# Kernel tuning notes

Measured on AMD Instinct MI355X. Metric: run time of the kernel, lower is better.

Reference implementation:

```python
import jax, jax.numpy as jnp
import numpy as np

RX, RY = 10, 10  # box filter half-widths (Angle == 0 path)


def setup_inputs() -> dict:
    key = jax.random.key(0)
    x = jax.random.normal(key, (8, 1, 2048, 2048), dtype=jnp.float32)
    # Angle == 0: constant all-ones box kernel (1,1,2rx+1,2ry+1), a fixed buffer
    kernelx = jnp.ones((1, 1, 2 * RX + 1, 2 * RY + 1), dtype=jnp.float32)
    return {"x": x, "kernelx": kernelx}


def reference(x, kernelx):
    # circular pad: H by rx (top/bottom), W by ry (left/right), matching
    # F.pad(input, (ry, ry, rx, rx), mode='circular')
    xp = jnp.pad(x, ((0, 0), (0, 0), (RX, RX), (RY, RY)), mode="wrap")
    # valid conv with the box kernel -> output has the original HxW
    out = jax.lax.conv_general_dilated(
        xp, kernelx,
        window_strides=(1, 1),
        padding="VALID",
        dimension_numbers=("NCHW", "OIHW", "NCHW"),
    )
    return out
```

## Files before the change

kernel.cpp:

```cpp
#include <hip/hip_runtime.h>


#define HH 2048
#define WW 2048
#define RAD 10
#define DIAM 21
#define TH 64
#define TW 64
#define CS_W (TW + 2 * RAD)
#define CS_STRIDE (CS_W + 1)

__global__ __launch_bounds__(256) void box_filter_v2(
    const float* __restrict__ x, float* __restrict__ out) {
  __shared__ float sCS[TH * CS_STRIDE];

  const int n = blockIdx.z;
  const int h0 = blockIdx.y * TH;
  const int w0 = blockIdx.x * TW;
  const float* __restrict__ xp = x + (size_t)n * HH * WW;
  float* __restrict__ op = out + (size_t)n * HH * WW;
  const int tid = threadIdx.x;

  for (int t = tid; t < CS_W * 4; t += 256) {
    int c = t % CS_W;
    int g = t / CS_W;
    int gc = (w0 - RAD + c) & (WW - 1);
    int rbase = h0 + 16 * g - RAD;
    float v[36];
#pragma unroll
    for (int k = 0; k < 36; ++k)
      v[k] = xp[(size_t)((rbase + k) & (HH - 1)) * WW + gc];
    float s = 0.f;
#pragma unroll
    for (int k = 0; k < DIAM; ++k) s += v[k];
    sCS[(16 * g) * CS_STRIDE + c] = s;
#pragma unroll
    for (int i = 1; i < 16; ++i) {
      s += v[i + DIAM - 1] - v[i - 1];
      sCS[(16 * g + i) * CS_STRIDE + c] = s;
    }
  }
  __syncthreads();

  {
    int r = tid >> 2;
    int cg = tid & 3;
    const float* csrow = &sCS[r * CS_STRIDE + cg * 16];
    float w[36];
#pragma unroll
    for (int k = 0; k < 36; ++k) w[k] = csrow[k];
    float o[16];
    float s = 0.f;
#pragma unroll
    for (int k = 0; k < DIAM; ++k) s += w[k];
    o[0] = s;
#pragma unroll
    for (int j = 1; j < 16; ++j) {
      s += w[j + DIAM - 1] - w[j - 1];
      o[j] = s;
    }
    float4* dst = (float4*)&op[(size_t)(h0 + r) * WW + w0 + cg * 16];
#pragma unroll
    for (int q = 0; q < 4; ++q)
      dst[q] = make_float4(o[4 * q], o[4 * q + 1], o[4 * q + 2], o[4 * q + 3]);
  }
}

extern "C" void kernel_launch(void* const* d_in, const int* in_sizes, int n_in,
                              void* d_out, int out_size, void* d_ws, size_t ws_size,
                              hipStream_t stream) {
  const float* x = (const float*)d_in[0];
  float* out = (float*)d_out;
  dim3 grid(WW / TW, HH / TH, 8);
  dim3 block(256);
  hipLaunchKernelGGL(box_filter_v2, grid, block, 0, stream, x, out);
}
```

Measured before the change: 261.8 us.

## Widen tile to 128 columns and vectorize vertical pass with float4 loads

The tile width doubles to 128 columns. The vertical sliding-sum pass now loads float4 columns, so each thread handles four columns and the 12-column aligned halo is read with 16-byte loads. The horizontal pass reads shared memory as float4 and computes two 16-wide output groups per thread. This cuts redundant halo reads and the number of scalar global loads, at the cost of much higher register use (36 float4 per thread) and 104 idle threads in the first phase.

```diff
diff --git a/kernel.cpp b/kernel.cpp
--- a/kernel.cpp
+++ b/kernel.cpp
@@ -6,63 +6,73 @@
 #define RAD 10
 #define DIAM 21
 #define TH 64
-#define TW 64
-#define CS_W (TW + 2 * RAD)
-#define CS_STRIDE (CS_W + 1)
+#define TW 128
+#define NC4 38
+#define SSTR 156
 
-__global__ __launch_bounds__(256) void box_filter_v2(
+__global__ __launch_bounds__(256) void box_filter_v3(
     const float* __restrict__ x, float* __restrict__ out) {
-  __shared__ float sCS[TH * CS_STRIDE];
+  __shared__ float sCS[TH * SSTR];
 
   const int n = blockIdx.z;
   const int h0 = blockIdx.y * TH;
   const int w0 = blockIdx.x * TW;
-  const float* __restrict__ xp = x + (size_t)n * HH * WW;
-  float* __restrict__ op = out + (size_t)n * HH * WW;
+  const float* __restrict__ xp = x + (size_t)n * (HH * WW);
+  float* __restrict__ op = out + (size_t)n * (HH * WW);
   const int tid = threadIdx.x;
 
-  for (int t = tid; t < CS_W * 4; t += 256) {
-    int c = t % CS_W;
-    int g = t / CS_W;
-    int gc = (w0 - RAD + c) & (WW - 1);
-    int rbase = h0 + 16 * g - RAD;
-    float v[36];
+  if (tid < NC4 * 4) {
+    const int c4 = tid % NC4;
+    const int g = tid / NC4;
+    const int gc = (w0 - 12 + 4 * c4) & (WW - 1);
+    const int rbase = h0 + 16 * g - RAD;
+    float4 v[36];
 #pragma unroll
     for (int k = 0; k < 36; ++k)
-      v[k] = xp[(size_t)((rbase + k) & (HH - 1)) * WW + gc];
-    float s = 0.f;
+      v[k] = *(const float4*)(xp + (size_t)((rbase + k) & (HH - 1)) * WW + gc);
+    float4 s = v[0];
 #pragma unroll
-    for (int k = 0; k < DIAM; ++k) s += v[k];
-    sCS[(16 * g) * CS_STRIDE + c] = s;
+    for (int k = 1; k < DIAM; ++k) {
+      s.x += v[k].x; s.y += v[k].y; s.z += v[k].z; s.w += v[k].w;
+    }
+    *(float4*)&sCS[(16 * g) * SSTR + 4 * c4] = s;
 #pragma unroll
     for (int i = 1; i < 16; ++i) {
-      s += v[i + DIAM - 1] - v[i - 1];
-      sCS[(16 * g + i) * CS_STRIDE + c] = s;
+      s.x += v[i + 20].x - v[i - 1].x;
+      s.y += v[i + 20].y - v[i - 1].y;
+      s.z += v[i + 20].z - v[i - 1].z;
+      s.w += v[i + 20].w - v[i - 1].w;
+      *(float4*)&sCS[(16 * g + i) * SSTR + 4 * c4] = s;
     }
   }
   __syncthreads();
 
   {
-    int r = tid >> 2;
-    int cg = tid & 3;
-    const float* csrow = &sCS[r * CS_STRIDE + cg * 16];
-    float w[36];
+    const int r = tid >> 2;
+    const float* row = &sCS[r * SSTR];
+    float* orow = &op[(size_t)(h0 + r) * WW + w0];
 #pragma unroll
-    for (int k = 0; k < 36; ++k) w[k] = csrow[k];
-    float o[16];
-    float s = 0.f;
+    for (int ii = 0; ii < 2; ++ii) {
+      const int cg = (tid & 3) + 4 * ii;
+      __align__(16) float w[40];
 #pragma unroll
-    for (int k = 0; k < DIAM; ++k) s += w[k];
-    o[0] = s;
+      for (int k = 0; k < 10; ++k)
+        *(float4*)&w[4 * k] = *(const float4*)&row[16 * cg + 4 * k];
+      float s = w[2];
 #pragma unroll
-    for (int j = 1; j < 16; ++j) {
-      s += w[j + DIAM - 1] - w[j - 1];
-      o[j] = s;
+      for (int k = 3; k <= 22; ++k) s += w[k];
+      float o[16];
+      o[0] = s;
+#pragma unroll
+      for (int j = 1; j < 16; ++j) {
+        s += w[j + 22] - w[j + 1];
+        o[j] = s;
+      }
+      float4* dst = (float4*)&orow[16 * cg];
+#pragma unroll
+      for (int q = 0; q < 4; ++q)
+        dst[q] = make_float4(o[4 * q], o[4 * q + 1], o[4 * q + 2], o[4 * q + 3]);
     }
-    float4* dst = (float4*)&op[(size_t)(h0 + r) * WW + w0 + cg * 16];
-#pragma unroll
-    for (int q = 0; q < 4; ++q)
-      dst[q] = make_float4(o[4 * q], o[4 * q + 1], o[4 * q + 2], o[4 * q + 3]);
   }
 }
 
@@ -73,5 +83,5 @@
   float* out = (float*)d_out;
   dim3 grid(WW / TW, HH / TH, 8);
   dim3 block(256);
-  hipLaunchKernelGGL(box_filter_v2, grid, block, 0, stream, x, out);
+  hipLaunchKernelGGL(box_filter_v3, grid, block, 0, stream, x, out);
 }
```

New measurement: 252.7 us. 3.5% less time.
